# Optimization experiments

Hardware: AMD Instinct MI355X
Metric: run time of the kernel (lower is better)

## Reference

```python
import jax, jax.numpy as jnp
import numpy as np

S_Q = 2048; B = 2; H = 16; D = 128
SCALE = 1.0 / np.sqrt(128.0)  # softmax_scale from init


def setup_inputs() -> dict:
    key = jax.random.key(0)
    kq, kk, kv, ks = jax.random.split(key, 4)
    q = jax.random.normal(kq, (S_Q, B, H, D), dtype=jnp.float32)
    k = jax.random.normal(kk, (S_Q, B, 1, D), dtype=jnp.float32)   # MQA: H_kv=1
    v = jax.random.normal(kv, (S_Q, B, 1, D), dtype=jnp.float32)
    sinks = jax.random.normal(ks, (H,), dtype=jnp.float32)         # learned per-head sink logits
    return {"q": q, "k": k, "v": v, "sinks": sinks, "mask": 0}


def reference(q, k, v, sinks, mask):
    # q: [S_q, B, H, D]; k, v: [S_k, B, H_kv, D] (H_kv may be 1 -> MQA expand)
    S_q, Bn, Hq, Dn = q.shape
    S_k = k.shape[0]
    k = jnp.broadcast_to(k, (S_k, Bn, Hq, Dn))
    v = jnp.broadcast_to(v, (S_k, Bn, Hq, Dn))
    # logits: [B, H, S_q, S_k]
    logits = jnp.einsum("sbhd,tbhd->bhst", q.astype(jnp.float32), k.astype(jnp.float32)) * SCALE
    # causal mask (triu(-inf, diag=1) added in original)
    causal = jnp.tril(jnp.ones((S_q, S_k), dtype=bool))
    logits = jnp.where(causal[None, None], logits, -jnp.inf)
    # sink-augmented softmax: append sink logit as extra column, softmax, drop it
    sink = sinks.astype(jnp.float32)[None, :, None, None]        # [1, H, 1, 1]
    m = jax.lax.stop_gradient(jnp.maximum(logits.max(axis=-1, keepdims=True), sink))
    e = jnp.exp(logits - m)                                      # [B, H, S_q, S_k]
    denom = e.sum(axis=-1, keepdims=True) + jnp.exp(sink - m)    # sink column contribution
    probs = e / denom
    out = jnp.einsum("bhst,tbhd->sbhd", probs.astype(v.dtype), v)  # [S_q, B, H, D]
    return out.reshape(S_q, Bn, Hq * Dn)
```

## Files before the change

### kernel.cpp

```cpp
#include <hip/hip_runtime.h>
#include <hip/hip_bf16.h>

#define SQ 2048
#define NBATCH 2
#define NHEAD 16
#define DHEAD 128
#define NKT 32
#define SCALE_L2E 0.1275174609f
#define LOG2E 1.4426950408889634f

typedef _Float16 f16x8 __attribute__((ext_vector_type(8)));
typedef _Float16 f16x4 __attribute__((ext_vector_type(4)));
typedef float f32x4 __attribute__((ext_vector_type(4)));

static __device__ __forceinline__ _Float16 f2h(float f) { return (_Float16)f; }

__global__ __launch_bounds__(256)
void prepack(const float* __restrict__ k, const float* __restrict__ v,
             _Float16* __restrict__ kws, _Float16* __restrict__ vws) {
    const int tile  = blockIdx.x;
    const int which = tile >> 6;
    const int b     = (tile >> 5) & 1;
    const int kt    = tile & 31;
    const int tid   = threadIdx.x;

    if (which == 0) {
        const float* kbase = k + (size_t)b * DHEAD + (size_t)kt * 64 * (NBATCH * DHEAD);
        _Float16* dst = kws + ((size_t)b * NKT + kt) * 8192;
        #pragma unroll
        for (int p = 0; p < 8; ++p) {
            const int id4 = tid + p * 256;
            const int row = id4 >> 5;
            const int c0  = (id4 & 31) << 2;
            f32x4 a = *(const f32x4*)(kbase + (size_t)row * (NBATCH * DHEAD) + c0);
            const int e = (row * 128 + c0) ^ ((row & 7) << 3);
            f16x4 pk = { f2h(a.x), f2h(a.y), f2h(a.z), f2h(a.w) };
            *(f16x4*)(dst + e) = pk;
        }
    } else {
        const float* vbase = v + (size_t)b * DHEAD;
        _Float16* dst = vws + ((size_t)b * NKT + kt) * 8192;
        const int d    = tid & 127;
        const int half = tid >> 7;
        #pragma unroll
        for (int p = 0; p < 8; ++p) {
            const int c0 = (p * 2 + half) * 4;
            float a0 = vbase[(size_t)(kt * 64 + c0 + 0) * (NBATCH * DHEAD) + d];
            float a1 = vbase[(size_t)(kt * 64 + c0 + 1) * (NBATCH * DHEAD) + d];
            float a2 = vbase[(size_t)(kt * 64 + c0 + 2) * (NBATCH * DHEAD) + d];
            float a3 = vbase[(size_t)(kt * 64 + c0 + 3) * (NBATCH * DHEAD) + d];
            const int e = (d * 64 + c0) ^ ((d & 7) << 3);
            f16x4 pk = { f2h(a0), f2h(a1), f2h(a2), f2h(a3) };
            *(f16x4*)(dst + e) = pk;
        }
    }
}

static __device__ __forceinline__ void gload16(const _Float16* gsrc, _Float16* ldst) {
    __builtin_amdgcn_global_load_lds(
        (const __attribute__((address_space(1))) void*)gsrc,
        (__attribute__((address_space(3))) void*)ldst, 16, 0, 0);
}

__global__ __launch_bounds__(256)
void attn_fwd(const float* __restrict__ q, const _Float16* __restrict__ kws,
              const _Float16* __restrict__ vws, const float* __restrict__ sinks,
              float* __restrict__ out) {
    __shared__ _Float16 Kb[2][8192];
    __shared__ _Float16 Vb[2][8192];
    __shared__ _Float16 Plds[4][16 * 64];

    const int tid  = threadIdx.x;
    const int w    = tid >> 6;
    const int lane = tid & 63;
    const int r    = lane & 15;
    const int g    = lane >> 4;

    const int bid = blockIdx.x;
    const int b   = bid & 1;
    const int h   = (bid >> 1) & 15;
    const int qt  = (NKT - 1) - (bid >> 5);
    const int q0  = qt * 64;
    const int sq  = q0 + w * 16 + r;

    f16x8 qf[4];
    {
        const float* qrow = q + ((size_t)sq * NBATCH + b) * (NHEAD * DHEAD) + h * DHEAD;
        #pragma unroll
        for (int kc = 0; kc < 4; ++kc) {
            const int d0 = kc * 32 + g * 8;
            f32x4 a = *(const f32x4*)(qrow + d0);
            f32x4 c = *(const f32x4*)(qrow + d0 + 4);
            f16x8 t;
            t[0] = f2h(a.x * SCALE_L2E); t[1] = f2h(a.y * SCALE_L2E);
            t[2] = f2h(a.z * SCALE_L2E); t[3] = f2h(a.w * SCALE_L2E);
            t[4] = f2h(c.x * SCALE_L2E); t[5] = f2h(c.y * SCALE_L2E);
            t[6] = f2h(c.z * SCALE_L2E); t[7] = f2h(c.w * SCALE_L2E);
            qf[kc] = t;
        }
    }

    float m_run = sinks[h] * LOG2E;
    float l_run = 1.0f;
    f32x4 acc[8];
    #pragma unroll
    for (int i = 0; i < 8; ++i) acc[i] = (f32x4)(0.0f);

    const _Float16* ktiles = kws + (size_t)b * NKT * 8192;
    const _Float16* vtiles = vws + (size_t)b * NKT * 8192;

    const int ntiles = qt + 1;

    #pragma unroll
    for (int j = 0; j < 4; ++j) {
        const int off = (w * 4 + j) * 512;
        gload16(ktiles + off + lane * 8, &Kb[0][off]);
        gload16(vtiles + off + lane * 8, &Vb[0][off]);
    }
    asm volatile("s_waitcnt vmcnt(0)" ::: "memory");
    __builtin_amdgcn_s_barrier();

    for (int it = 0; it < ntiles; ++it) {
        const int cur = it & 1;
        if (it + 1 < ntiles) {
            const _Float16* kt_n = ktiles + (size_t)(it + 1) * 8192;
            const _Float16* vt_n = vtiles + (size_t)(it + 1) * 8192;
            #pragma unroll
            for (int j = 0; j < 4; ++j) {
                const int off = (w * 4 + j) * 512;
                gload16(kt_n + off + lane * 8, &Kb[cur ^ 1][off]);
                gload16(vt_n + off + lane * 8, &Vb[cur ^ 1][off]);
            }
        }

        float s[16];
        #pragma unroll
        for (int ct = 0; ct < 4; ++ct) {
            f32x4 sa = (f32x4)(0.0f);
            const int c = ct * 16 + r;
            #pragma unroll
            for (int kc = 0; kc < 4; ++kc) {
                const int e = (c * 128 + kc * 32 + g * 8) ^ ((c & 7) << 3);
                f16x8 kf = *(const f16x8*)(&Kb[cur][e]);
                sa = __builtin_amdgcn_mfma_f32_16x16x32_f16(kf, qf[kc], sa, 0, 0, 0);
            }
            #pragma unroll
            for (int i = 0; i < 4; ++i) s[ct * 4 + i] = sa[i];
        }

        if (it == qt) {
            #pragma unroll
            for (int ct = 0; ct < 4; ++ct)
                #pragma unroll
                for (int i = 0; i < 4; ++i) {
                    const int tk = q0 + ct * 16 + g * 4 + i;
                    if (tk > sq) s[ct * 4 + i] = -1e30f;
                }
        }

        float mx = s[0];
        #pragma unroll
        for (int i = 1; i < 16; ++i) mx = fmaxf(mx, s[i]);
        mx = fmaxf(mx, __shfl_xor(mx, 16));
        mx = fmaxf(mx, __shfl_xor(mx, 32));
        const float mnew = fmaxf(m_run, mx);
        const float corr = __builtin_amdgcn_exp2f(m_run - mnew);
        m_run = mnew;

        float ls = 0.0f;
        #pragma unroll
        for (int i = 0; i < 16; ++i) {
            const float p = __builtin_amdgcn_exp2f(s[i] - mnew);
            s[i] = p;
            ls += p;
        }
        ls += __shfl_xor(ls, 16);
        ls += __shfl_xor(ls, 32);
        l_run = l_run * corr + ls;

        #pragma unroll
        for (int i = 0; i < 4; ++i) {
            const float ci = __shfl(corr, (lane & 48) | (g * 4 + i));
            #pragma unroll
            for (int nb = 0; nb < 8; ++nb) acc[nb][i] *= ci;
        }

        #pragma unroll
        for (int t = 0; t < 4; ++t) {
            f16x4 pb = { f2h(s[t * 4 + 0]), f2h(s[t * 4 + 1]),
                         f2h(s[t * 4 + 2]), f2h(s[t * 4 + 3]) };
            const int c0 = t * 16 + g * 4;
            const int e = (r * 64 + c0) ^ ((r & 7) << 3);
            *(f16x4*)(&Plds[w][e]) = pb;
        }

        #pragma unroll
        for (int cc = 0; cc < 2; ++cc) {
            const int ep = (r * 64 + cc * 32 + g * 8) ^ ((r & 7) << 3);
            f16x8 pf = *(const f16x8*)(&Plds[w][ep]);
            #pragma unroll
            for (int nb = 0; nb < 8; ++nb) {
                const int d = nb * 16 + r;
                const int ev = (d * 64 + cc * 32 + g * 8) ^ ((d & 7) << 3);
                f16x8 vf = *(const f16x8*)(&Vb[cur][ev]);
                acc[nb] = __builtin_amdgcn_mfma_f32_16x16x32_f16(pf, vf, acc[nb], 0, 0, 0);
            }
        }

        asm volatile("s_waitcnt vmcnt(0)" ::: "memory");
        __builtin_amdgcn_s_barrier();
        asm volatile("" ::: "memory");
    }

    #pragma unroll
    for (int i = 0; i < 4; ++i) {
        const float li = __shfl(l_run, (lane & 48) | (g * 4 + i));
        const float rl = 1.0f / li;
        const int row = q0 + w * 16 + g * 4 + i;
        float* op = out + ((size_t)row * NBATCH + b) * (NHEAD * DHEAD) + h * DHEAD + r;
        #pragma unroll
        for (int nb = 0; nb < 8; ++nb)
            op[nb * 16] = acc[nb][i] * rl;
    }
}

extern "C" void kernel_launch(void* const* d_in, const int* in_sizes, int n_in,
                              void* d_out, int out_size, void* d_ws, size_t ws_size,
                              hipStream_t stream) {
    const float* q     = (const float*)d_in[0];
    const float* k     = (const float*)d_in[1];
    const float* v     = (const float*)d_in[2];
    const float* sinks = (const float*)d_in[3];
    float* out = (float*)d_out;

    _Float16* kws = (_Float16*)d_ws;
    _Float16* vws = kws + (size_t)NBATCH * NKT * 8192;

    prepack<<<dim3(128), 256, 0, stream>>>(k, v, kws, vws);
    attn_fwd<<<dim3(NKT * NBATCH * NHEAD), 256, 0, stream>>>(q, kws, vws, sinks, out);
}
```

Baseline: 78.38 us.

## Use 32x32 MFMA with 128-row query tiles, register P, and deferred rescale

Each block now covers 128 query rows, with 32 rows per wave, using 32x32x16 MFMAs in place of 16x16x32. The probability matrix stays in registers through cvt_pkrtz packing and permlane32 swaps, so the LDS round trip for P is gone. The online-softmax rescale is skipped unless the new max exceeds the running max by a threshold, and waves skip fully masked K tiles. This halves the block count and raises per-block register pressure, and the deferred max risks fp16 overflow if the threshold is set badly.

```diff
diff --git a/kernel.cpp b/kernel.cpp
--- a/kernel.cpp
+++ b/kernel.cpp
@@ -6,14 +6,24 @@
 #define NHEAD 16
 #define DHEAD 128
 #define NKT 32
+#define NQT 16
 #define SCALE_L2E 0.1275174609f
 #define LOG2E 1.4426950408889634f
+#define DEFER_THR 11.0f
 
 typedef _Float16 f16x8 __attribute__((ext_vector_type(8)));
 typedef _Float16 f16x4 __attribute__((ext_vector_type(4)));
+typedef __fp16 fp16x2 __attribute__((ext_vector_type(2)));
 typedef float f32x4 __attribute__((ext_vector_type(4)));
+typedef float f32x16 __attribute__((ext_vector_type(16)));
+typedef unsigned int u32x4 __attribute__((ext_vector_type(4)));
 
 static __device__ __forceinline__ _Float16 f2h(float f) { return (_Float16)f; }
+
+static __device__ __forceinline__ unsigned int pkrtz(float a, float b) {
+    fp16x2 h = __builtin_amdgcn_cvt_pkrtz(a, b);
+    return __builtin_bit_cast(unsigned int, h);
+}
 
 __global__ __launch_bounds__(256)
 void prepack(const float* __restrict__ k, const float* __restrict__ v,
@@ -68,27 +78,26 @@
               float* __restrict__ out) {
     __shared__ _Float16 Kb[2][8192];
     __shared__ _Float16 Vb[2][8192];
-    __shared__ _Float16 Plds[4][16 * 64];
 
     const int tid  = threadIdx.x;
     const int w    = tid >> 6;
     const int lane = tid & 63;
-    const int r    = lane & 15;
-    const int g    = lane >> 4;
+    const int qc   = lane & 31;
+    const int h2   = lane >> 5;
 
     const int bid = blockIdx.x;
     const int b   = bid & 1;
     const int h   = (bid >> 1) & 15;
-    const int qt  = (NKT - 1) - (bid >> 5);
-    const int q0  = qt * 64;
-    const int sq  = q0 + w * 16 + r;
-
-    f16x8 qf[4];
+    const int qt  = (NQT - 1) - (bid >> 5);
+    const int q0  = qt * 128;
+    const int sq  = q0 + w * 32 + qc;
+
+    f16x8 qf[8];
     {
         const float* qrow = q + ((size_t)sq * NBATCH + b) * (NHEAD * DHEAD) + h * DHEAD;
         #pragma unroll
-        for (int kc = 0; kc < 4; ++kc) {
-            const int d0 = kc * 32 + g * 8;
+        for (int ks = 0; ks < 8; ++ks) {
+            const int d0 = ks * 16 + h2 * 8;
             f32x4 a = *(const f32x4*)(qrow + d0);
             f32x4 c = *(const f32x4*)(qrow + d0 + 4);
             f16x8 t;
@@ -96,20 +105,19 @@
             t[2] = f2h(a.z * SCALE_L2E); t[3] = f2h(a.w * SCALE_L2E);
             t[4] = f2h(c.x * SCALE_L2E); t[5] = f2h(c.y * SCALE_L2E);
             t[6] = f2h(c.z * SCALE_L2E); t[7] = f2h(c.w * SCALE_L2E);
-            qf[kc] = t;
+            qf[ks] = t;
         }
     }
 
     float m_run = sinks[h] * LOG2E;
     float l_run = 1.0f;
-    f32x4 acc[8];
+    f32x16 acc[4];
     #pragma unroll
-    for (int i = 0; i < 8; ++i) acc[i] = (f32x4)(0.0f);
+    for (int i = 0; i < 4; ++i) acc[i] = (f32x16)(0.0f);
 
     const _Float16* ktiles = kws + (size_t)b * NKT * 8192;
     const _Float16* vtiles = vws + (size_t)b * NKT * 8192;
-
-    const int ntiles = qt + 1;
+    const int ntiles = 2 * qt + 2;
 
     #pragma unroll
     for (int j = 0; j < 4; ++j) {
@@ -133,95 +141,106 @@
             }
         }
 
-        float s[16];
-        #pragma unroll
-        for (int ct = 0; ct < 4; ++ct) {
-            f32x4 sa = (f32x4)(0.0f);
-            const int c = ct * 16 + r;
-            #pragma unroll
-            for (int kc = 0; kc < 4; ++kc) {
-                const int e = (c * 128 + kc * 32 + g * 8) ^ ((c & 7) << 3);
-                f16x8 kf = *(const f16x8*)(&Kb[cur][e]);
-                sa = __builtin_amdgcn_mfma_f32_16x16x32_f16(kf, qf[kc], sa, 0, 0, 0);
-            }
-            #pragma unroll
-            for (int i = 0; i < 4; ++i) s[ct * 4 + i] = sa[i];
-        }
-
-        if (it == qt) {
-            #pragma unroll
-            for (int ct = 0; ct < 4; ++ct)
-                #pragma unroll
-                for (int i = 0; i < 4; ++i) {
-                    const int tk = q0 + ct * 16 + g * 4 + i;
-                    if (tk > sq) s[ct * 4 + i] = -1e30f;
+        const int ktbase = it * 64;
+        if (ktbase <= q0 + w * 32 + 31) {
+            f32x16 sa0 = (f32x16)(0.0f), sa1 = (f32x16)(0.0f);
+            #pragma unroll
+            for (int ks = 0; ks < 8; ++ks) {
+                const int col = ks * 16 + h2 * 8;
+                const int e0 = (qc * 128 + col) ^ ((qc & 7) << 3);
+                const int e1 = ((32 + qc) * 128 + col) ^ ((qc & 7) << 3);
+                f16x8 k0 = *(const f16x8*)(&Kb[cur][e0]);
+                f16x8 k1 = *(const f16x8*)(&Kb[cur][e1]);
+                sa0 = __builtin_amdgcn_mfma_f32_32x32x16_f16(k0, qf[ks], sa0, 0, 0, 0);
+                sa1 = __builtin_amdgcn_mfma_f32_32x32x16_f16(k1, qf[ks], sa1, 0, 0, 0);
+            }
+
+            float sv[32];
+            #pragma unroll
+            for (int i = 0; i < 16; ++i) { sv[i] = sa0[i]; sv[16 + i] = sa1[i]; }
+
+            if (ktbase + 63 > q0 + w * 32) {
+                #pragma unroll
+                for (int mt = 0; mt < 2; ++mt)
+                    #pragma unroll
+                    for (int i = 0; i < 16; ++i) {
+                        const int tk = ktbase + (i & 3) + 8 * (i >> 2) + 4 * h2 + 32 * mt;
+                        if (tk > sq) sv[mt * 16 + i] = -1e30f;
+                    }
+            }
+
+            float mx = sv[0];
+            #pragma unroll
+            for (int i = 1; i < 32; ++i) mx = fmaxf(mx, sv[i]);
+            mx = fmaxf(mx, __shfl_xor(mx, 32));
+
+            if (!__all(mx <= m_run + DEFER_THR)) {
+                const float mnew = fmaxf(m_run, mx);
+                const float corr = __builtin_amdgcn_exp2f(m_run - mnew);
+                m_run = mnew;
+                l_run *= corr;
+                #pragma unroll
+                for (int mt = 0; mt < 4; ++mt) acc[mt] *= corr;
+            }
+
+            float ls = 0.0f;
+            #pragma unroll
+            for (int i = 0; i < 32; ++i) {
+                const float p = __builtin_amdgcn_exp2f(sv[i] - m_run);
+                sv[i] = p;
+                ls += p;
+            }
+            ls += __shfl_xor(ls, 32);
+            l_run += ls;
+
+            unsigned int pw[4][4];
+            #pragma unroll
+            for (int mt = 0; mt < 2; ++mt) {
+                unsigned int e0[4], e1[4];
+                #pragma unroll
+                for (int bq = 0; bq < 4; ++bq) {
+                    e0[bq] = pkrtz(sv[mt * 16 + 4 * bq + 0], sv[mt * 16 + 4 * bq + 1]);
+                    e1[bq] = pkrtz(sv[mt * 16 + 4 * bq + 2], sv[mt * 16 + 4 * bq + 3]);
                 }
-        }
-
-        float mx = s[0];
-        #pragma unroll
-        for (int i = 1; i < 16; ++i) mx = fmaxf(mx, s[i]);
-        mx = fmaxf(mx, __shfl_xor(mx, 16));
-        mx = fmaxf(mx, __shfl_xor(mx, 32));
-        const float mnew = fmaxf(m_run, mx);
-        const float corr = __builtin_amdgcn_exp2f(m_run - mnew);
-        m_run = mnew;
-
-        float ls = 0.0f;
-        #pragma unroll
-        for (int i = 0; i < 16; ++i) {
-            const float p = __builtin_amdgcn_exp2f(s[i] - mnew);
-            s[i] = p;
-            ls += p;
-        }
-        ls += __shfl_xor(ls, 16);
-        ls += __shfl_xor(ls, 32);
-        l_run = l_run * corr + ls;
-
-        #pragma unroll
-        for (int i = 0; i < 4; ++i) {
-            const float ci = __shfl(corr, (lane & 48) | (g * 4 + i));
-            #pragma unroll
-            for (int nb = 0; nb < 8; ++nb) acc[nb][i] *= ci;
-        }
-
-        #pragma unroll
-        for (int t = 0; t < 4; ++t) {
-            f16x4 pb = { f2h(s[t * 4 + 0]), f2h(s[t * 4 + 1]),
-                         f2h(s[t * 4 + 2]), f2h(s[t * 4 + 3]) };
-            const int c0 = t * 16 + g * 4;
-            const int e = (r * 64 + c0) ^ ((r & 7) << 3);
-            *(f16x4*)(&Plds[w][e]) = pb;
-        }
-
-        #pragma unroll
-        for (int cc = 0; cc < 2; ++cc) {
-            const int ep = (r * 64 + cc * 32 + g * 8) ^ ((r & 7) << 3);
-            f16x8 pf = *(const f16x8*)(&Plds[w][ep]);
-            #pragma unroll
-            for (int nb = 0; nb < 8; ++nb) {
-                const int d = nb * 16 + r;
-                const int ev = (d * 64 + cc * 32 + g * 8) ^ ((d & 7) << 3);
-                f16x8 vf = *(const f16x8*)(&Vb[cur][ev]);
-                acc[nb] = __builtin_amdgcn_mfma_f32_16x16x32_f16(pf, vf, acc[nb], 0, 0, 0);
+                #pragma unroll
+                for (int kl = 0; kl < 2; ++kl) {
+                    unsigned int a0 = e0[2 * kl], b0 = e0[2 * kl + 1];
+                    unsigned int a1 = e1[2 * kl], b1 = e1[2 * kl + 1];
+                    asm volatile("v_permlane32_swap_b32 %0, %1" : "+v"(a0), "+v"(b0));
+                    asm volatile("v_permlane32_swap_b32 %0, %1" : "+v"(a1), "+v"(b1));
+                    pw[mt * 2 + kl][0] = a0; pw[mt * 2 + kl][1] = a1;
+                    pw[mt * 2 + kl][2] = b0; pw[mt * 2 + kl][3] = b1;
+                }
+            }
+
+            #pragma unroll
+            for (int ks = 0; ks < 4; ++ks) {
+                u32x4 pu = { pw[ks][0], pw[ks][1], pw[ks][2], pw[ks][3] };
+                f16x8 pf = __builtin_bit_cast(f16x8, pu);
+                #pragma unroll
+                for (int mt = 0; mt < 4; ++mt) {
+                    const int d = mt * 32 + qc;
+                    const int e = (d * 64 + ks * 16 + h2 * 8) ^ ((qc & 7) << 3);
+                    f16x8 vf = *(const f16x8*)(&Vb[cur][e]);
+                    acc[mt] = __builtin_amdgcn_mfma_f32_32x32x16_f16(vf, pf, acc[mt], 0, 0, 0);
+                }
             }
         }
 
         asm volatile("s_waitcnt vmcnt(0)" ::: "memory");
         __builtin_amdgcn_s_barrier();
-        asm volatile("" ::: "memory");
-    }
-
+    }
+
+    const float rl = 1.0f / l_run;
+    float* orow = out + ((size_t)sq * NBATCH + b) * (NHEAD * DHEAD) + h * DHEAD;
     #pragma unroll
-    for (int i = 0; i < 4; ++i) {
-        const float li = __shfl(l_run, (lane & 48) | (g * 4 + i));
-        const float rl = 1.0f / li;
-        const int row = q0 + w * 16 + g * 4 + i;
-        float* op = out + ((size_t)row * NBATCH + b) * (NHEAD * DHEAD) + h * DHEAD + r;
-        #pragma unroll
-        for (int nb = 0; nb < 8; ++nb)
-            op[nb * 16] = acc[nb][i] * rl;
-    }
+    for (int mt = 0; mt < 4; ++mt)
+        #pragma unroll
+        for (int rg = 0; rg < 4; ++rg) {
+            f32x4 o = { acc[mt][4 * rg + 0] * rl, acc[mt][4 * rg + 1] * rl,
+                        acc[mt][4 * rg + 2] * rl, acc[mt][4 * rg + 3] * rl };
+            *(f32x4*)(orow + mt * 32 + rg * 8 + h2 * 4) = o;
+        }
 }
 
 extern "C" void kernel_launch(void* const* d_in, const int* in_sizes, int n_in,
@@ -237,5 +256,5 @@
     _Float16* vws = kws + (size_t)NBATCH * NKT * 8192;
 
     prepack<<<dim3(128), 256, 0, stream>>>(k, v, kws, vws);
-    attn_fwd<<<dim3(NKT * NBATCH * NHEAD), 256, 0, stream>>>(q, kws, vws, sinks, out);
-}
+    attn_fwd<<<dim3(NQT * NBATCH * NHEAD), 256, 0, stream>>>(q, kws, vws, sinks, out);
+}
```

Result: slower. 85.14 us (+8.6%).

## Use 32-key tiles with per-wave causal skip, lazy rescale, and interleaved tile order

Applied to the files above, without the earlier changes.

Halves the KV tile to 32 keys so each wave can skip fully masked tiles and mask only tiles on the diagonal. The online softmax rescale is deferred until the running max grows past a threshold, which removes most accumulator rescales. Query tiles are scheduled in a zig-zag order and occupancy is hinted to 4 blocks per CU, with less shared memory per block. In exchange there are twice as many loop iterations and barriers, and the deferred rescale lets exponentials exceed 1 (bounded by 2^11) before conversion to fp16.

```diff
diff --git a/kernel.cpp b/kernel.cpp
--- a/kernel.cpp
+++ b/kernel.cpp
@@ -1,13 +1,14 @@
 #include <hip/hip_runtime.h>
-#include <hip/hip_bf16.h>
 
 #define SQ 2048
-#define NBATCH 2
-#define NHEAD 16
-#define DHEAD 128
-#define NKT 32
+#define NB 2
+#define NH 16
+#define DH 128
+#define NT32 64
+#define NQT 32
 #define SCALE_L2E 0.1275174609f
 #define LOG2E 1.4426950408889634f
+#define DEFER_THR 11.0f
 
 typedef _Float16 f16x8 __attribute__((ext_vector_type(8)));
 typedef _Float16 f16x4 __attribute__((ext_vector_type(4)));
@@ -18,38 +19,38 @@
 __global__ __launch_bounds__(256)
 void prepack(const float* __restrict__ k, const float* __restrict__ v,
              _Float16* __restrict__ kws, _Float16* __restrict__ vws) {
-    const int tile  = blockIdx.x;
-    const int which = tile >> 6;
-    const int b     = (tile >> 5) & 1;
-    const int kt    = tile & 31;
+    const int bid   = blockIdx.x;
+    const int which = bid >> 7;
+    const int b     = (bid >> 6) & 1;
+    const int t     = bid & 63;
     const int tid   = threadIdx.x;
 
     if (which == 0) {
-        const float* kbase = k + (size_t)b * DHEAD + (size_t)kt * 64 * (NBATCH * DHEAD);
-        _Float16* dst = kws + ((size_t)b * NKT + kt) * 8192;
-        #pragma unroll
-        for (int p = 0; p < 8; ++p) {
-            const int id4 = tid + p * 256;
+        const float* kbase = k + (size_t)t * 32 * (NB * DH) + b * DH;
+        _Float16* dst = kws + ((size_t)b * NT32 + t) * 4096;
+        #pragma unroll
+        for (int p = 0; p < 4; ++p) {
+            const int id4 = p * 256 + tid;
             const int row = id4 >> 5;
             const int c0  = (id4 & 31) << 2;
-            f32x4 a = *(const f32x4*)(kbase + (size_t)row * (NBATCH * DHEAD) + c0);
+            f32x4 a = *(const f32x4*)(kbase + (size_t)row * (NB * DH) + c0);
             const int e = (row * 128 + c0) ^ ((row & 7) << 3);
             f16x4 pk = { f2h(a.x), f2h(a.y), f2h(a.z), f2h(a.w) };
             *(f16x4*)(dst + e) = pk;
         }
     } else {
-        const float* vbase = v + (size_t)b * DHEAD;
-        _Float16* dst = vws + ((size_t)b * NKT + kt) * 8192;
+        const float* vbase = v + b * DH;
+        _Float16* dst = vws + ((size_t)b * NT32 + t) * 4096;
         const int d    = tid & 127;
         const int half = tid >> 7;
         #pragma unroll
-        for (int p = 0; p < 8; ++p) {
+        for (int p = 0; p < 4; ++p) {
             const int c0 = (p * 2 + half) * 4;
-            float a0 = vbase[(size_t)(kt * 64 + c0 + 0) * (NBATCH * DHEAD) + d];
-            float a1 = vbase[(size_t)(kt * 64 + c0 + 1) * (NBATCH * DHEAD) + d];
-            float a2 = vbase[(size_t)(kt * 64 + c0 + 2) * (NBATCH * DHEAD) + d];
-            float a3 = vbase[(size_t)(kt * 64 + c0 + 3) * (NBATCH * DHEAD) + d];
-            const int e = (d * 64 + c0) ^ ((d & 7) << 3);
+            float a0 = vbase[(size_t)(t * 32 + c0 + 0) * (NB * DH) + d];
+            float a1 = vbase[(size_t)(t * 32 + c0 + 1) * (NB * DH) + d];
+            float a2 = vbase[(size_t)(t * 32 + c0 + 2) * (NB * DH) + d];
+            float a3 = vbase[(size_t)(t * 32 + c0 + 3) * (NB * DH) + d];
+            const int e = (d * 32 + c0) ^ ((d & 7) << 3);
             f16x4 pk = { f2h(a0), f2h(a1), f2h(a2), f2h(a3) };
             *(f16x4*)(dst + e) = pk;
         }
@@ -62,13 +63,13 @@
         (__attribute__((address_space(3))) void*)ldst, 16, 0, 0);
 }
 
-__global__ __launch_bounds__(256)
+__global__ __launch_bounds__(256, 4)
 void attn_fwd(const float* __restrict__ q, const _Float16* __restrict__ kws,
               const _Float16* __restrict__ vws, const float* __restrict__ sinks,
               float* __restrict__ out) {
-    __shared__ _Float16 Kb[2][8192];
-    __shared__ _Float16 Vb[2][8192];
-    __shared__ _Float16 Plds[4][16 * 64];
+    __shared__ _Float16 Kb[2][4096];
+    __shared__ _Float16 Vb[2][4096];
+    __shared__ _Float16 Plds[4][512];
 
     const int tid  = threadIdx.x;
     const int w    = tid >> 6;
@@ -76,16 +77,21 @@
     const int r    = lane & 15;
     const int g    = lane >> 4;
 
-    const int bid = blockIdx.x;
-    const int b   = bid & 1;
-    const int h   = (bid >> 1) & 15;
-    const int qt  = (NKT - 1) - (bid >> 5);
-    const int q0  = qt * 64;
-    const int sq  = q0 + w * 16 + r;
+    const int bid   = blockIdx.x;
+    const int bh    = bid & 31;
+    const int b     = bh & 1;
+    const int h     = bh >> 1;
+    const int qtIdx = bid >> 5;
+    const int jj    = qtIdx & 7;
+    const int mm    = qtIdx >> 3;
+    const int qt = (mm == 0) ? jj : (mm == 1) ? 15 - jj
+                 : (mm == 2) ? 16 + jj : 31 - jj;
+    const int q0 = qt * 64;
+    const int sq = q0 + w * 16 + r;
 
     f16x8 qf[4];
     {
-        const float* qrow = q + ((size_t)sq * NBATCH + b) * (NHEAD * DHEAD) + h * DHEAD;
+        const float* qrow = q + ((size_t)sq * NB + b) * (NH * DH) + h * DH;
         #pragma unroll
         for (int kc = 0; kc < 4; ++kc) {
             const int d0 = kc * 32 + g * 8;
@@ -106,16 +112,16 @@
     #pragma unroll
     for (int i = 0; i < 8; ++i) acc[i] = (f32x4)(0.0f);
 
-    const _Float16* ktiles = kws + (size_t)b * NKT * 8192;
-    const _Float16* vtiles = vws + (size_t)b * NKT * 8192;
-
-    const int ntiles = qt + 1;
+    const _Float16* ktiles = kws + (size_t)b * NT32 * 4096;
+    const _Float16* vtiles = vws + (size_t)b * NT32 * 4096;
+    const int ntiles = 2 * qt + 2;
+    const int wlimit = q0 + w * 16 + 15;
 
     #pragma unroll
-    for (int j = 0; j < 4; ++j) {
-        const int off = (w * 4 + j) * 512;
-        gload16(ktiles + off + lane * 8, &Kb[0][off]);
-        gload16(vtiles + off + lane * 8, &Vb[0][off]);
+    for (int p = 0; p < 2; ++p) {
+        const int off = (p * 256 + tid) * 8;
+        gload16(ktiles + off, &Kb[0][off]);
+        gload16(vtiles + off, &Vb[0][off]);
     }
     asm volatile("s_waitcnt vmcnt(0)" ::: "memory");
     __builtin_amdgcn_s_barrier();
@@ -123,85 +129,87 @@
     for (int it = 0; it < ntiles; ++it) {
         const int cur = it & 1;
         if (it + 1 < ntiles) {
-            const _Float16* kt_n = ktiles + (size_t)(it + 1) * 8192;
-            const _Float16* vt_n = vtiles + (size_t)(it + 1) * 8192;
-            #pragma unroll
-            for (int j = 0; j < 4; ++j) {
-                const int off = (w * 4 + j) * 512;
-                gload16(kt_n + off + lane * 8, &Kb[cur ^ 1][off]);
-                gload16(vt_n + off + lane * 8, &Vb[cur ^ 1][off]);
-            }
-        }
-
-        float s[16];
-        #pragma unroll
-        for (int ct = 0; ct < 4; ++ct) {
-            f32x4 sa = (f32x4)(0.0f);
-            const int c = ct * 16 + r;
-            #pragma unroll
-            for (int kc = 0; kc < 4; ++kc) {
-                const int e = (c * 128 + kc * 32 + g * 8) ^ ((c & 7) << 3);
-                f16x8 kf = *(const f16x8*)(&Kb[cur][e]);
-                sa = __builtin_amdgcn_mfma_f32_16x16x32_f16(kf, qf[kc], sa, 0, 0, 0);
-            }
-            #pragma unroll
-            for (int i = 0; i < 4; ++i) s[ct * 4 + i] = sa[i];
-        }
-
-        if (it == qt) {
-            #pragma unroll
-            for (int ct = 0; ct < 4; ++ct)
+            const _Float16* kn = ktiles + (size_t)(it + 1) * 4096;
+            const _Float16* vn = vtiles + (size_t)(it + 1) * 4096;
+            #pragma unroll
+            for (int p = 0; p < 2; ++p) {
+                const int off = (p * 256 + tid) * 8;
+                gload16(kn + off, &Kb[cur ^ 1][off]);
+                gload16(vn + off, &Vb[cur ^ 1][off]);
+            }
+        }
+
+        const int ktb = it * 32;
+        if (ktb <= wlimit) {
+            float sv[8];
+            #pragma unroll
+            for (int ct = 0; ct < 2; ++ct) {
+                f32x4 sa = (f32x4)(0.0f);
+                const int c = ct * 16 + r;
+                #pragma unroll
+                for (int kc = 0; kc < 4; ++kc) {
+                    const int e = (c * 128 + kc * 32 + g * 8) ^ ((c & 7) << 3);
+                    f16x8 kf = *(const f16x8*)(&Kb[cur][e]);
+                    sa = __builtin_amdgcn_mfma_f32_16x16x32_f16(kf, qf[kc], sa, 0, 0, 0);
+                }
+                #pragma unroll
+                for (int i = 0; i < 4; ++i) sv[ct * 4 + i] = sa[i];
+            }
+
+            if (ktb + 31 > q0 + w * 16) {
+                #pragma unroll
+                for (int ct = 0; ct < 2; ++ct)
+                    #pragma unroll
+                    for (int i = 0; i < 4; ++i) {
+                        const int tk = ktb + ct * 16 + g * 4 + i;
+                        if (tk > sq) sv[ct * 4 + i] = -1e30f;
+                    }
+            }
+
+            float a0 = fmaxf(sv[0], sv[1]), a1 = fmaxf(sv[2], sv[3]);
+            float a2 = fmaxf(sv[4], sv[5]), a3 = fmaxf(sv[6], sv[7]);
+            float mx = fmaxf(fmaxf(a0, a1), fmaxf(a2, a3));
+            mx = fmaxf(mx, __shfl_xor(mx, 16));
+            mx = fmaxf(mx, __shfl_xor(mx, 32));
+
+            if (!__all(mx <= m_run + DEFER_THR)) {
+                const float mnew = fmaxf(m_run, mx);
+                const float corr = __builtin_amdgcn_exp2f(m_run - mnew);
+                m_run = mnew;
+                l_run *= corr;
                 #pragma unroll
                 for (int i = 0; i < 4; ++i) {
-                    const int tk = q0 + ct * 16 + g * 4 + i;
-                    if (tk > sq) s[ct * 4 + i] = -1e30f;
+                    const float ci = __shfl(corr, (lane & 48) | (g * 4 + i));
+                    #pragma unroll
+                    for (int nb = 0; nb < 8; ++nb) acc[nb][i] *= ci;
                 }
-        }
-
-        float mx = s[0];
-        #pragma unroll
-        for (int i = 1; i < 16; ++i) mx = fmaxf(mx, s[i]);
-        mx = fmaxf(mx, __shfl_xor(mx, 16));
-        mx = fmaxf(mx, __shfl_xor(mx, 32));
-        const float mnew = fmaxf(m_run, mx);
-        const float corr = __builtin_amdgcn_exp2f(m_run - mnew);
-        m_run = mnew;
-
-        float ls = 0.0f;
-        #pragma unroll
-        for (int i = 0; i < 16; ++i) {
-            const float p = __builtin_amdgcn_exp2f(s[i] - mnew);
-            s[i] = p;
-            ls += p;
-        }
-        ls += __shfl_xor(ls, 16);
-        ls += __shfl_xor(ls, 32);
-        l_run = l_run * corr + ls;
-
-        #pragma unroll
-        for (int i = 0; i < 4; ++i) {
-            const float ci = __shfl(corr, (lane & 48) | (g * 4 + i));
-            #pragma unroll
-            for (int nb = 0; nb < 8; ++nb) acc[nb][i] *= ci;
-        }
-
-        #pragma unroll
-        for (int t = 0; t < 4; ++t) {
-            f16x4 pb = { f2h(s[t * 4 + 0]), f2h(s[t * 4 + 1]),
-                         f2h(s[t * 4 + 2]), f2h(s[t * 4 + 3]) };
-            const int c0 = t * 16 + g * 4;
-            const int e = (r * 64 + c0) ^ ((r & 7) << 3);
-            *(f16x4*)(&Plds[w][e]) = pb;
-        }
-
-        #pragma unroll
-        for (int cc = 0; cc < 2; ++cc) {
-            const int ep = (r * 64 + cc * 32 + g * 8) ^ ((r & 7) << 3);
+            }
+
+            #pragma unroll
+            for (int i = 0; i < 8; ++i)
+                sv[i] = __builtin_amdgcn_exp2f(sv[i] - m_run);
+            float s0 = (sv[0] + sv[1]) + (sv[2] + sv[3]);
+            float s1 = (sv[4] + sv[5]) + (sv[6] + sv[7]);
+            float ls = s0 + s1;
+            ls += __shfl_xor(ls, 16);
+            ls += __shfl_xor(ls, 32);
+            l_run += ls;
+
+            #pragma unroll
+            for (int ct = 0; ct < 2; ++ct) {
+                f16x4 pb = { f2h(sv[ct * 4 + 0]), f2h(sv[ct * 4 + 1]),
+                             f2h(sv[ct * 4 + 2]), f2h(sv[ct * 4 + 3]) };
+                const int c0 = ct * 16 + g * 4;
+                const int e = (r * 32 + c0) ^ ((r & 7) << 3);
+                *(f16x4*)(&Plds[w][e]) = pb;
+            }
+
+            const int ep = (r * 32 + g * 8) ^ ((r & 7) << 3);
             f16x8 pf = *(const f16x8*)(&Plds[w][ep]);
             #pragma unroll
             for (int nb = 0; nb < 8; ++nb) {
                 const int d = nb * 16 + r;
-                const int ev = (d * 64 + cc * 32 + g * 8) ^ ((d & 7) << 3);
+                const int ev = (d * 32 + g * 8) ^ ((d & 7) << 3);
                 f16x8 vf = *(const f16x8*)(&Vb[cur][ev]);
                 acc[nb] = __builtin_amdgcn_mfma_f32_16x16x32_f16(pf, vf, acc[nb], 0, 0, 0);
             }
@@ -209,7 +217,6 @@
 
         asm volatile("s_waitcnt vmcnt(0)" ::: "memory");
         __builtin_amdgcn_s_barrier();
-        asm volatile("" ::: "memory");
     }
 
     #pragma unroll
@@ -217,7 +224,7 @@
         const float li = __shfl(l_run, (lane & 48) | (g * 4 + i));
         const float rl = 1.0f / li;
         const int row = q0 + w * 16 + g * 4 + i;
-        float* op = out + ((size_t)row * NBATCH + b) * (NHEAD * DHEAD) + h * DHEAD + r;
+        float* op = out + ((size_t)row * NB + b) * (NH * DH) + h * DH + r;
         #pragma unroll
         for (int nb = 0; nb < 8; ++nb)
             op[nb * 16] = acc[nb][i] * rl;
@@ -234,8 +241,8 @@
     float* out = (float*)d_out;
 
     _Float16* kws = (_Float16*)d_ws;
-    _Float16* vws = kws + (size_t)NBATCH * NKT * 8192;
-
-    prepack<<<dim3(128), 256, 0, stream>>>(k, v, kws, vws);
-    attn_fwd<<<dim3(NKT * NBATCH * NHEAD), 256, 0, stream>>>(q, kws, vws, sinks, out);
-}
+    _Float16* vws = kws + (size_t)NB * NT32 * 4096;
+
+    prepack<<<dim3(256), 256, 0, stream>>>(k, v, kws, vws);
+    attn_fwd<<<dim3(NQT * NB * NH), 256, 0, stream>>>(q, kws, vws, sinks, out);
+}
```

Measured after the change: 89.60 us. +14.3%, slower.
